# Performance work log

Measured on AMD Instinct MI355X. Metric: run time of the kernel, lower is better.

The kernel has to match this reference:

```python
import jax, jax.numpy as jnp
import numpy as np

N_NODES = 50000


def gcn_conv(x, W, b, src, dst, n_nodes):
    """PyG GCNConv: add self-loops, symmetric norm, linear, scatter-add, bias."""
    h = x @ W  # [N, out]
    # degree with self-loops: deg[i] = 1 + (# edges with dst == i)
    deg = 1.0 + jax.ops.segment_sum(jnp.ones_like(dst, dtype=h.dtype), dst,
                                    num_segments=n_nodes)
    dinv = jax.lax.rsqrt(deg)  # deg^{-1/2}
    # per-edge norm for non-self-loop edges
    norm = dinv[src] * dinv[dst]  # [E]
    agg = jax.ops.segment_sum(h[src] * norm[:, None], dst,
                              num_segments=n_nodes)
    # self-loop contribution: dinv[i]*dinv[i]*h[i] = h[i]/deg[i]
    agg = agg + h * (dinv * dinv)[:, None]
    return agg + b


def setup_inputs() -> dict:
    key = jax.random.key(0)
    ks = jax.random.split(key, 6)
    x = jax.random.normal(ks[0], (N_NODES, 512), dtype=jnp.float32)
    edge_index = jax.random.randint(ks[1], (2, 800000), 0, N_NODES,
                                    dtype=jnp.int64)
    W1 = jax.random.normal(ks[2], (512, 256), dtype=jnp.float32) * (512 ** -0.5)
    b1 = jnp.zeros((256,), dtype=jnp.float32)
    W2 = jax.random.normal(ks[3], (256, 256), dtype=jnp.float32) * (256 ** -0.5)
    b2 = jnp.zeros((256,), dtype=jnp.float32)
    W3 = jax.random.normal(ks[4], (256, 64), dtype=jnp.float32) * (256 ** -0.5)
    b3 = jnp.zeros((64,), dtype=jnp.float32)
    return {"x": x, "edge_index": edge_index, "W1": W1, "b1": b1,
            "W2": W2, "b2": b2, "W3": W3, "b3": b3}


def reference(x, edge_index, W1, b1, W2, b2, W3, b3):
    src, dst = edge_index[0], edge_index[1]
    n = x.shape[0]
    h = gcn_conv(x, W1, b1, src, dst, n)
    h = jax.nn.relu(h)  # dropout is a no-op in eval mode
    h = gcn_conv(h, W2, b2, src, dst, n)
    h = jax.nn.relu(h)
    h = gcn_conv(h, W3, b3, src, dst, n)
    # faithful to the original: softmax then log_softmax
    h = jax.nn.softmax(h, axis=1)
    return jax.nn.log_softmax(h, axis=1)
```

## Files before the change

### kernel.cpp

```cpp
#include <hip/hip_runtime.h>
#include <cstdint>
#include <cstddef>

typedef float  f32x4  __attribute__((ext_vector_type(4)));
typedef float  f32x2  __attribute__((ext_vector_type(2)));

__device__ __forceinline__ unsigned int f2fp8x4(float a, float b, float c, float d) {
  int v = __builtin_amdgcn_cvt_pk_fp8_f32(a, b, 0, false);
  v = __builtin_amdgcn_cvt_pk_fp8_f32(c, d, v, true);
  return (unsigned int)v;
}
__device__ __forceinline__ unsigned char f2fp8(float f) {
  return (unsigned char)(__builtin_amdgcn_cvt_pk_fp8_f32(f, f, 0, false) & 0xff);
}
__device__ __forceinline__ void fp8x8_to_f32(uint2 d, float* f) {
  f32x2 a = __builtin_amdgcn_cvt_pk_f32_fp8((int)d.x, false);
  f32x2 b = __builtin_amdgcn_cvt_pk_f32_fp8((int)d.x, true);
  f32x2 c = __builtin_amdgcn_cvt_pk_f32_fp8((int)d.y, false);
  f32x2 e = __builtin_amdgcn_cvt_pk_f32_fp8((int)d.y, true);
  f[0] = a.x; f[1] = a.y; f[2] = b.x; f[3] = b.y;
  f[4] = c.x; f[5] = c.y; f[6] = e.x; f[7] = e.y;
}
__device__ __forceinline__ void fp8x4_to_f32(unsigned int d, float* f) {
  f32x2 a = __builtin_amdgcn_cvt_pk_f32_fp8((int)d, false);
  f32x2 b = __builtin_amdgcn_cvt_pk_f32_fp8((int)d, true);
  f[0] = a.x; f[1] = a.y; f[2] = b.x; f[3] = b.y;
}
__device__ __forceinline__ void fp8x16_to_f32(uint4 d, float* f) {
  uint2 lo; lo.x = d.x; lo.y = d.y;
  uint2 hi; hi.x = d.z; hi.y = d.w;
  fp8x8_to_f32(lo, f);
  fp8x8_to_f32(hi, f + 8);
}

__device__ __forceinline__ void async_copy16(const void* g, void* l) {
  __builtin_amdgcn_global_load_lds(
      (const __attribute__((address_space(1))) unsigned int*)g,
      (__attribute__((address_space(3))) unsigned int*)l, 16, 0, 0);
}

#define NN 50000
#define MPAD 50048
#define SCAN_BLOCKS 196

#define XB_BLOCKS 6256
#define WB_BLOCKS 52

__global__ __launch_bounds__(256) void gcn_prep_k(
    const float* __restrict__ X, unsigned char* __restrict__ x8,
    const float* __restrict__ W1, const float* __restrict__ W2,
    const float* __restrict__ W3,
    unsigned char* __restrict__ W1T8, unsigned char* __restrict__ W2T8,
    unsigned char* __restrict__ W3T8, int* __restrict__ cnt) {
  int b = blockIdx.x;
  if (b < SCAN_BLOCKS) {
    int ii = b * 256 + threadIdx.x;
    if (ii < NN) cnt[ii] = 0;
  }
  if (b < XB_BLOCKS) {
    int idx16 = (b * 256 + threadIdx.x) * 16;
    int row = idx16 >> 9;
    uint4 o;
    if (row < NN) {
      const float* s = &X[idx16];
      float4 v0 = *(const float4*)s;
      float4 v1 = *(const float4*)(s + 4);
      float4 v2 = *(const float4*)(s + 8);
      float4 v3 = *(const float4*)(s + 12);
      o.x = f2fp8x4(v0.x, v0.y, v0.z, v0.w);
      o.y = f2fp8x4(v1.x, v1.y, v1.z, v1.w);
      o.z = f2fp8x4(v2.x, v2.y, v2.z, v2.w);
      o.w = f2fp8x4(v3.x, v3.y, v3.z, v3.w);
    } else {
      o = uint4{0, 0, 0, 0};
    }
    *(uint4*)&x8[idx16] = o;
  } else {
    int wb = b - XB_BLOCKS;
    if (wb < 32) {
      int idx16 = (wb * 256 + threadIdx.x) * 16;
      int n = idx16 >> 9;
      float f[16];
#pragma unroll
      for (int j = 0; j < 16; j++) f[j] = W1[(size_t)((idx16 & 511) + j) * 256 + n];
      uint4 o;
      o.x = f2fp8x4(f[0], f[1], f[2], f[3]);
      o.y = f2fp8x4(f[4], f[5], f[6], f[7]);
      o.z = f2fp8x4(f[8], f[9], f[10], f[11]);
      o.w = f2fp8x4(f[12], f[13], f[14], f[15]);
      *(uint4*)&W1T8[idx16] = o;
    } else if (wb < 48) {
      int idx16 = ((wb - 32) * 256 + threadIdx.x) * 16;
      int n = idx16 >> 8;
      float f[16];
#pragma unroll
      for (int j = 0; j < 16; j++) f[j] = W2[(size_t)((idx16 & 255) + j) * 256 + n];
      uint4 o;
      o.x = f2fp8x4(f[0], f[1], f[2], f[3]);
      o.y = f2fp8x4(f[4], f[5], f[6], f[7]);
      o.z = f2fp8x4(f[8], f[9], f[10], f[11]);
      o.w = f2fp8x4(f[12], f[13], f[14], f[15]);
      *(uint4*)&W2T8[idx16] = o;
    } else {
      int idx16 = ((wb - 48) * 256 + threadIdx.x) * 16;
      int n = idx16 >> 8;
      float f[16];
#pragma unroll
      for (int j = 0; j < 16; j++) f[j] = W3[(size_t)((idx16 & 255) + j) * 64 + n];
      uint4 o;
      o.x = f2fp8x4(f[0], f[1], f[2], f[3]);
      o.y = f2fp8x4(f[4], f[5], f[6], f[7]);
      o.z = f2fp8x4(f[8], f[9], f[10], f[11]);
      o.w = f2fp8x4(f[12], f[13], f[14], f[15]);
      *(uint4*)&W3T8[idx16] = o;
    }
  }
}

__global__ void gcn_count_k(const int* __restrict__ dst, int* __restrict__ cnt,
                            int* __restrict__ rank, int E) {
  int e = blockIdx.x * 256 + threadIdx.x;
  if (e < E) rank[e] = atomicAdd(&cnt[dst[e]], 1);
}

__global__ __launch_bounds__(256) void gcn_scan_blocks_k(
    const int* __restrict__ cnt, int* __restrict__ blockSum, int nNodes) {
  __shared__ int sw[4];
  int t = threadIdx.x;
  int i = blockIdx.x * 256 + t;
  int v = (i < nNodes) ? cnt[i] : 0;
  for (int off = 32; off > 0; off >>= 1) v += __shfl_down(v, off);
  if ((t & 63) == 0) sw[t >> 6] = v;
  __syncthreads();
  if (t == 0) blockSum[blockIdx.x] = sw[0] + sw[1] + sw[2] + sw[3];
}

__global__ __launch_bounds__(256) void gcn_scan_tops_k(
    int* __restrict__ blockSum, int nBlocks) {
  __shared__ int sb[256];
  int t = threadIdx.x;
  int v = (t < nBlocks) ? blockSum[t] : 0;
  sb[t] = v;
  __syncthreads();
  for (int off = 1; off < 256; off <<= 1) {
    int x = (t >= off) ? sb[t - off] : 0;
    __syncthreads();
    sb[t] += x;
    __syncthreads();
  }
  if (t < nBlocks) blockSum[t] = sb[t] - v;
}

__global__ __launch_bounds__(256) void gcn_scan_final_k(
    const int* __restrict__ cnt, const int* __restrict__ blockSum,
    int* __restrict__ rs, float* __restrict__ dinv, int nNodes, int E) {
  __shared__ int sb[256];
  int t = threadIdx.x;
  int i = blockIdx.x * 256 + t;
  int v = (i < nNodes) ? cnt[i] : 0;
  sb[t] = v;
  __syncthreads();
  for (int off = 1; off < 256; off <<= 1) {
    int x = (t >= off) ? sb[t - off] : 0;
    __syncthreads();
    sb[t] += x;
    __syncthreads();
  }
  if (i < nNodes) {
    rs[i] = blockSum[blockIdx.x] + sb[t] - v;
    dinv[i] = rsqrtf(1.0f + (float)v);
  } else if (i < MPAD) {
    dinv[i] = 0.0f;
  }
  if (i == 0) rs[nNodes] = E;
}

__global__ void gcn_scatter_k(const int* __restrict__ src, const int* __restrict__ dst,
                              const int* __restrict__ rank, const int* __restrict__ rs,
                              int* __restrict__ e4, int E) {
  int e = blockIdx.x * 256 + threadIdx.x;
  if (e < E) {
    int d = dst[e];
    e4[rs[d] + rank[e]] = src[e];
  }
}

template<int BN, int WTN>
__global__ __launch_bounds__(256) void gcn_gemm_f8_db_k(
    const unsigned char* __restrict__ A8,
    const unsigned char* __restrict__ Bt8,
    const float* __restrict__ dinv,
    unsigned char* __restrict__ C8,
    int K, int N) {
  static_assert(BN == 128, "db kernel assumes uniform 2 global_load_lds per thread");
  __shared__ __align__(16) unsigned char lds_a[2][128 * 32];
  __shared__ __align__(16) unsigned char lds_b[2][BN * 32];
  const int t = threadIdx.x;
  const int wave = t >> 6, lane = t & 63;
  const int wr = wave >> 1, wc = wave & 1;
  const int quad = lane >> 4, lrow = lane & 15;
  const int m0 = blockIdx.x * 128;
  const int n0 = blockIdx.y * BN;

  f32x4 acc[4][WTN] = {};

  auto stage = [&](int buf, int k0) {
    int r = t >> 1, c = (t & 1) * 16;
    async_copy16(&A8[(size_t)(m0 + r) * K + k0 + c], &lds_a[buf][t * 16]);
    async_copy16(&Bt8[(size_t)(n0 + r) * K + k0 + c], &lds_b[buf][t * 16]);
  };
  auto compute = [&](int buf) {
    long af[4], bfr[WTN];
#pragma unroll
    for (int mt = 0; mt < 4; mt++)
      af[mt] = *(const long*)&lds_a[buf][(wr * 64 + mt * 16 + lrow) * 32 + quad * 8];
#pragma unroll
    for (int nt = 0; nt < WTN; nt++)
      bfr[nt] = *(const long*)&lds_b[buf][(wc * (BN / 2) + nt * 16 + lrow) * 32 + quad * 8];
#pragma unroll
    for (int mt = 0; mt < 4; mt++)
#pragma unroll
      for (int nt = 0; nt < WTN; nt++)
        acc[mt][nt] = __builtin_amdgcn_mfma_f32_16x16x32_fp8_fp8(af[mt], bfr[nt], acc[mt][nt], 0, 0, 0);
  };

  stage(0, 0);
  int curb = 0;
  int k0 = 0;
  for (; k0 + 32 < K; k0 += 32) {
    stage(curb ^ 1, k0 + 32);
    asm volatile("s_waitcnt vmcnt(2)" ::: "memory");
    __builtin_amdgcn_s_barrier();
    asm volatile("" ::: "memory");
    compute(curb);
    asm volatile("" ::: "memory");
    __builtin_amdgcn_s_barrier();
    curb ^= 1;
  }
  asm volatile("s_waitcnt vmcnt(0)" ::: "memory");
  __builtin_amdgcn_s_barrier();
  asm volatile("" ::: "memory");
  compute(curb);

#pragma unroll
  for (int mt = 0; mt < 4; mt++)
#pragma unroll
    for (int r = 0; r < 4; r++) {
      int row = m0 + wr * 64 + mt * 16 + quad * 4 + r;
      float dv = dinv[row];
#pragma unroll
      for (int nt = 0; nt < WTN; nt++) {
        int col = n0 + wc * (BN / 2) + nt * 16 + lrow;
        C8[(size_t)row * N + col] = f2fp8(acc[mt][nt][r] * dv);
      }
    }
}

template<int BN, int WTN>
__global__ __launch_bounds__(256) void gcn_gemm_f8_s_k(
    const unsigned char* __restrict__ A8, const unsigned char* __restrict__ Bt8,
    const float* __restrict__ dinv, unsigned char* __restrict__ C8, int K, int N) {
  __shared__ __align__(16) unsigned char lds_a[128 * 32];
  __shared__ __align__(16) unsigned char lds_b[BN * 32];
  const int t = threadIdx.x;
  const int wave = t >> 6, lane = t & 63;
  const int wr = wave >> 1, wc = wave & 1;
  const int quad = lane >> 4, lrow = lane & 15;
  const int m0 = blockIdx.x * 128;
  const int n0 = blockIdx.y * BN;

  f32x4 acc[4][WTN] = {};

  for (int k0 = 0; k0 < K; k0 += 32) {
    __syncthreads();
    {
      int r = t >> 1, c = (t & 1) * 16;
      async_copy16(&A8[(size_t)(m0 + r) * K + k0 + c], &lds_a[t * 16]);
    }
    for (int q = t; q < BN * 2; q += 256) {
      int r = q >> 1, c = (q & 1) * 16;
      async_copy16(&Bt8[(size_t)(n0 + r) * K + k0 + c], &lds_b[q * 16]);
    }
    __syncthreads();
    long af[4], bfr[WTN];
#pragma unroll
    for (int mt = 0; mt < 4; mt++)
      af[mt] = *(const long*)&lds_a[(wr * 64 + mt * 16 + lrow) * 32 + quad * 8];
#pragma unroll
    for (int nt = 0; nt < WTN; nt++)
      bfr[nt] = *(const long*)&lds_b[(wc * (BN / 2) + nt * 16 + lrow) * 32 + quad * 8];
#pragma unroll
    for (int mt = 0; mt < 4; mt++)
#pragma unroll
      for (int nt = 0; nt < WTN; nt++)
        acc[mt][nt] = __builtin_amdgcn_mfma_f32_16x16x32_fp8_fp8(af[mt], bfr[nt], acc[mt][nt], 0, 0, 0);
  }

#pragma unroll
  for (int mt = 0; mt < 4; mt++)
#pragma unroll
    for (int r = 0; r < 4; r++) {
      int row = m0 + wr * 64 + mt * 16 + quad * 4 + r;
      float dv = dinv[row];
#pragma unroll
      for (int nt = 0; nt < WTN; nt++) {
        int col = n0 + wc * (BN / 2) + nt * 16 + lrow;
        C8[(size_t)row * N + col] = f2fp8(acc[mt][nt][r] * dv);
      }
    }
}

template<int D>
__global__ __launch_bounds__(256) void gcn_agg_relu_k(
    const unsigned char* __restrict__ g8, const int* __restrict__ rs,
    const int* __restrict__ e4, const float* __restrict__ dinv,
    const float* __restrict__ bias, unsigned char* __restrict__ out8, int nNodes) {
  int wave = threadIdx.x >> 6, lane = threadIdx.x & 63;
  int i = blockIdx.x * 4 + wave;
  if (i >= nNodes) return;
  int q = lane >> 4, sub = lane & 15;
  int f0 = sub * 16;
  float di = dinv[i];
  uint4 dself = *(const uint4*)&g8[(size_t)i * D + f0];
  float sv[16];
  fp8x16_to_f32(dself, sv);
  float wself = (q == 0) ? 1.0f : 0.0f;
  float acc[16];
#pragma unroll
  for (int j = 0; j < 16; j++) acc[j] = sv[j] * wself;

  int e0 = rs[i], e1 = rs[i + 1];
  int nIter = (e1 - e0 + 15) >> 4;
  int e = e0 + q;
  for (int k = 0; k < nIter; k++) {
    int idx[4]; float w[4];
#pragma unroll
    for (int u = 0; u < 4; u++) {
      int ee = e + 4 * u;
      bool v = ee < e1;
      idx[u] = v ? e4[ee] : 0;
      w[u] = v ? 1.0f : 0.0f;
    }
    uint4 d0 = *(const uint4*)&g8[(size_t)idx[0] * D + f0];
    uint4 d1 = *(const uint4*)&g8[(size_t)idx[1] * D + f0];
    uint4 d2 = *(const uint4*)&g8[(size_t)idx[2] * D + f0];
    uint4 d3 = *(const uint4*)&g8[(size_t)idx[3] * D + f0];
    float r[16];
    fp8x16_to_f32(d0, r);
#pragma unroll
    for (int j = 0; j < 16; j++) acc[j] += r[j] * w[0];
    fp8x16_to_f32(d1, r);
#pragma unroll
    for (int j = 0; j < 16; j++) acc[j] += r[j] * w[1];
    fp8x16_to_f32(d2, r);
#pragma unroll
    for (int j = 0; j < 16; j++) acc[j] += r[j] * w[2];
    fp8x16_to_f32(d3, r);
#pragma unroll
    for (int j = 0; j < 16; j++) acc[j] += r[j] * w[3];
    e += 16;
  }
#pragma unroll
  for (int j = 0; j < 16; j++) {
    acc[j] += __shfl_xor(acc[j], 16);
    acc[j] += __shfl_xor(acc[j], 32);
  }
  if (q == 0) {
    float4 bb0 = *(const float4*)&bias[f0];
    float4 bb1 = *(const float4*)&bias[f0 + 4];
    float4 bb2 = *(const float4*)&bias[f0 + 8];
    float4 bb3 = *(const float4*)&bias[f0 + 12];
    float bv[16] = {bb0.x, bb0.y, bb0.z, bb0.w, bb1.x, bb1.y, bb1.z, bb1.w,
                    bb2.x, bb2.y, bb2.z, bb2.w, bb3.x, bb3.y, bb3.z, bb3.w};
    float r[16];
#pragma unroll
    for (int j = 0; j < 16; j++) {
      float z = di * acc[j] + bv[j];
      r[j] = z > 0.0f ? z : 0.0f;
    }
    uint4 o;
    o.x = f2fp8x4(r[0], r[1], r[2], r[3]);
    o.y = f2fp8x4(r[4], r[5], r[6], r[7]);
    o.z = f2fp8x4(r[8], r[9], r[10], r[11]);
    o.w = f2fp8x4(r[12], r[13], r[14], r[15]);
    *(uint4*)&out8[(size_t)i * D + f0] = o;
  }
}

__global__ __launch_bounds__(256) void gcn_agg_final_k(
    const unsigned char* __restrict__ g8, const int* __restrict__ rs,
    const int* __restrict__ e4, const float* __restrict__ dinv,
    const float* __restrict__ bias, float* __restrict__ out, int nNodes) {
  int wave = threadIdx.x >> 6, lane = threadIdx.x & 63;
  int i = blockIdx.x * 4 + wave;
  if (i >= nNodes) return;
  int qtr = lane >> 4, sub = lane & 15;
  int f0 = sub * 4;
  float di = dinv[i];
  unsigned int dself = *(const unsigned int*)&g8[(size_t)i * 64 + f0];
  float sv[4];
  fp8x4_to_f32(dself, sv);
  float wself = (qtr == 0) ? 1.0f : 0.0f;
  float acc[4];
#pragma unroll
  for (int j = 0; j < 4; j++) acc[j] = sv[j] * wself;

  int e0 = rs[i], e1 = rs[i + 1];
  int nIter = (e1 - e0 + 7) >> 3;
  int e = e0 + qtr;
  for (int k = 0; k < nIter; k++) {
    int idx[2]; float w[2];
#pragma unroll
    for (int u = 0; u < 2; u++) {
      int ee = e + 4 * u;
      bool v = ee < e1;
      idx[u] = v ? e4[ee] : 0;
      w[u] = v ? 1.0f : 0.0f;
    }
    unsigned int d0 = *(const unsigned int*)&g8[(size_t)idx[0] * 64 + f0];
    unsigned int d1 = *(const unsigned int*)&g8[(size_t)idx[1] * 64 + f0];
    float r0[4], r1[4];
    fp8x4_to_f32(d0, r0); fp8x4_to_f32(d1, r1);
#pragma unroll
    for (int j = 0; j < 4; j++)
      acc[j] += r0[j] * w[0] + r1[j] * w[1];
    e += 8;
  }
#pragma unroll
  for (int j = 0; j < 4; j++) {
    acc[j] += __shfl_xor(acc[j], 16);
    acc[j] += __shfl_xor(acc[j], 32);
    acc[j] = di * acc[j] + bias[f0 + j];
  }
  float m = fmaxf(fmaxf(acc[0], acc[1]), fmaxf(acc[2], acc[3]));
#pragma unroll
  for (int off = 8; off > 0; off >>= 1) m = fmaxf(m, __shfl_xor(m, off));
  float ex[4], s = 0.0f;
#pragma unroll
  for (int j = 0; j < 4; j++) { ex[j] = __expf(acc[j] - m); s += ex[j]; }
#pragma unroll
  for (int off = 8; off > 0; off >>= 1) s += __shfl_xor(s, off);
  float rcs = 1.0f / s;
  float p[4], s2 = 0.0f;
#pragma unroll
  for (int j = 0; j < 4; j++) { p[j] = ex[j] * rcs; s2 += __expf(p[j]); }
#pragma unroll
  for (int off = 8; off > 0; off >>= 1) s2 += __shfl_xor(s2, off);
  float ls = __logf(s2);
  if (qtr == 0) {
    float4 o; o.x = p[0] - ls; o.y = p[1] - ls; o.z = p[2] - ls; o.w = p[3] - ls;
    *(float4*)&out[(size_t)i * 64 + f0] = o;
  }
}

extern "C" void kernel_launch(void* const* d_in, const int* in_sizes, int n_in,
                              void* d_out, int out_size, void* d_ws, size_t ws_size,
                              hipStream_t stream) {
  const float* x    = (const float*)d_in[0];
  const int*   eidx = (const int*)d_in[1];
  const float* W1   = (const float*)d_in[2];
  const float* b1   = (const float*)d_in[3];
  const float* W2   = (const float*)d_in[4];
  const float* b2   = (const float*)d_in[5];
  const float* W3   = (const float*)d_in[6];
  const float* b3   = (const float*)d_in[7];
  float* out = (float*)d_out;

  const int E = in_sizes[1] / 2;
  const int* src = eidx;
  const int* dst = eidx + E;

  char* p = (char*)d_ws;
  auto alloc = [&](size_t bytes) -> void* {
    void* r = (void*)p;
    p += (bytes + 255) & ~(size_t)255;
    return r;
  };
  unsigned char*  x8   = (unsigned char*)alloc((size_t)MPAD * 512);
  unsigned char*  g8   = (unsigned char*)alloc((size_t)MPAD * 256);
  unsigned char*  a8   = (unsigned char*)alloc((size_t)MPAD * 256);
  unsigned char*  g83  = (unsigned char*)alloc((size_t)MPAD * 64);
  unsigned char*  W1T8 = (unsigned char*)alloc((size_t)256 * 512);
  unsigned char*  W2T8 = (unsigned char*)alloc((size_t)256 * 256);
  unsigned char*  W3T8 = (unsigned char*)alloc((size_t)64 * 256);
  int*   cnt  = (int*)alloc((size_t)NN * 4);
  int*   rs   = (int*)alloc((size_t)(NN + 1) * 4);
  int*   rank = (int*)alloc((size_t)E * 4);
  float* dinv = (float*)alloc((size_t)MPAD * 4);
  int*   e4   = (int*)alloc((size_t)(E + 64) * 4);
  int*   bsum = (int*)alloc((size_t)SCAN_BLOCKS * 4);

  const int EB = (E + 255) / 256;
  gcn_prep_k<<<XB_BLOCKS + WB_BLOCKS, 256, 0, stream>>>(
      x, x8, W1, W2, W3, W1T8, W2T8, W3T8, cnt);
  gcn_count_k<<<EB, 256, 0, stream>>>(dst, cnt, rank, E);
  gcn_scan_blocks_k<<<SCAN_BLOCKS, 256, 0, stream>>>(cnt, bsum, NN);
  gcn_scan_tops_k<<<1, 256, 0, stream>>>(bsum, SCAN_BLOCKS);
  gcn_scan_final_k<<<SCAN_BLOCKS, 256, 0, stream>>>(cnt, bsum, rs, dinv, NN, E);
  gcn_scatter_k<<<EB, 256, 0, stream>>>(src, dst, rank, rs, e4, E);

  const int MB = MPAD / 128;
  gcn_gemm_f8_db_k<128, 4><<<dim3(MB, 2), 256, 0, stream>>>(x8, W1T8, dinv, g8, 512, 256);
  gcn_agg_relu_k<256><<<(NN + 3) / 4, 256, 0, stream>>>(g8, rs, e4, dinv, b1, a8, NN);
  gcn_gemm_f8_db_k<128, 4><<<dim3(MB, 2), 256, 0, stream>>>(a8, W2T8, dinv, g8, 256, 256);
  gcn_agg_relu_k<256><<<(NN + 3) / 4, 256, 0, stream>>>(g8, rs, e4, dinv, b2, a8, NN);
  gcn_gemm_f8_s_k<64, 2><<<dim3(MB, 1), 256, 0, stream>>>(a8, W3T8, dinv, g83, 256, 64);
  gcn_agg_final_k<<<(NN + 3) / 4, 256, 0, stream>>>(g83, rs, e4, dinv, b3, out, NN);

  (void)n_in; (void)out_size; (void)ws_size;
}
```

Measured before the change: 406.7 us.

## Fuse first GEMM with edge-count kernel and fold top-level scan into final scan

The first-layer GEMM no longer depends on dinv: the source-side dinv scaling moves into the first aggregation kernel, which now reads dinv per neighbour. That lets GEMM1 run in the same launch as the edge-degree atomic counting, so compute-heavy and atomic-heavy blocks share the GPU. The single-block top-level scan kernel is removed, and every final-scan block instead re-scans the block sums redundantly. The cost is an extra dinv gather per edge in layer-1 aggregation and duplicated scan work in each block.

```diff
diff --git a/kernel.cpp b/kernel.cpp
--- a/kernel.cpp
+++ b/kernel.cpp
@@ -45,6 +45,9 @@
 
 #define XB_BLOCKS 6256
 #define WB_BLOCKS 52
+
+#define GEMM1_BLOCKS 782
+#define COUNT_BLOCKS 3125
 
 __global__ __launch_bounds__(256) void gcn_prep_k(
     const float* __restrict__ X, unsigned char* __restrict__ x8,
@@ -117,10 +120,77 @@
   }
 }
 
-__global__ void gcn_count_k(const int* __restrict__ dst, int* __restrict__ cnt,
-                            int* __restrict__ rank, int E) {
-  int e = blockIdx.x * 256 + threadIdx.x;
-  if (e < E) rank[e] = atomicAdd(&cnt[dst[e]], 1);
+__global__ __launch_bounds__(256) void gcn_gemm1_count_k(
+    const unsigned char* __restrict__ A8,
+    const unsigned char* __restrict__ Bt8,
+    unsigned char* __restrict__ C8,
+    const int* __restrict__ dst, int* __restrict__ cnt, int* __restrict__ rank, int E) {
+  __shared__ __align__(16) unsigned char lds_a[2][128 * 32];
+  __shared__ __align__(16) unsigned char lds_b[2][128 * 32];
+  int b = blockIdx.x;
+  if (b >= GEMM1_BLOCKS) {
+    int e = (b - GEMM1_BLOCKS) * 256 + threadIdx.x;
+    if (e < E) rank[e] = atomicAdd(&cnt[dst[e]], 1);
+    return;
+  }
+  const int K = 512, N = 256;
+  const int t = threadIdx.x;
+  const int wave = t >> 6, lane = t & 63;
+  const int wr = wave >> 1, wc = wave & 1;
+  const int quad = lane >> 4, lrow = lane & 15;
+  const int m0 = (b >> 1) * 128;
+  const int n0 = (b & 1) * 128;
+
+  f32x4 acc[4][4] = {};
+
+  auto stage = [&](int buf, int k0) {
+    int r = t >> 1, c = (t & 1) * 16;
+    async_copy16(&A8[(size_t)(m0 + r) * K + k0 + c], &lds_a[buf][t * 16]);
+    async_copy16(&Bt8[(size_t)(n0 + r) * K + k0 + c], &lds_b[buf][t * 16]);
+  };
+  auto compute = [&](int buf) {
+    long af[4], bfr[4];
+#pragma unroll
+    for (int mt = 0; mt < 4; mt++)
+      af[mt] = *(const long*)&lds_a[buf][(wr * 64 + mt * 16 + lrow) * 32 + quad * 8];
+#pragma unroll
+    for (int nt = 0; nt < 4; nt++)
+      bfr[nt] = *(const long*)&lds_b[buf][(wc * 64 + nt * 16 + lrow) * 32 + quad * 8];
+#pragma unroll
+    for (int mt = 0; mt < 4; mt++)
+#pragma unroll
+      for (int nt = 0; nt < 4; nt++)
+        acc[mt][nt] = __builtin_amdgcn_mfma_f32_16x16x32_fp8_fp8(af[mt], bfr[nt], acc[mt][nt], 0, 0, 0);
+  };
+
+  stage(0, 0);
+  int curb = 0;
+  int k0 = 0;
+  for (; k0 + 32 < K; k0 += 32) {
+    stage(curb ^ 1, k0 + 32);
+    asm volatile("s_waitcnt vmcnt(2)" ::: "memory");
+    __builtin_amdgcn_s_barrier();
+    asm volatile("" ::: "memory");
+    compute(curb);
+    asm volatile("" ::: "memory");
+    __builtin_amdgcn_s_barrier();
+    curb ^= 1;
+  }
+  asm volatile("s_waitcnt vmcnt(0)" ::: "memory");
+  __builtin_amdgcn_s_barrier();
+  asm volatile("" ::: "memory");
+  compute(curb);
+
+#pragma unroll
+  for (int mt = 0; mt < 4; mt++)
+#pragma unroll
+    for (int nt = 0; nt < 4; nt++)
+#pragma unroll
+      for (int r = 0; r < 4; r++) {
+        int row = m0 + wr * 64 + mt * 16 + quad * 4 + r;
+        int col = n0 + wc * 64 + nt * 16 + lrow;
+        C8[(size_t)row * N + col] = f2fp8(acc[mt][nt][r]);
+      }
 }
 
 __global__ __launch_bounds__(256) void gcn_scan_blocks_k(
@@ -135,39 +205,29 @@
   if (t == 0) blockSum[blockIdx.x] = sw[0] + sw[1] + sw[2] + sw[3];
 }
 
-__global__ __launch_bounds__(256) void gcn_scan_tops_k(
-    int* __restrict__ blockSum, int nBlocks) {
-  __shared__ int sb[256];
-  int t = threadIdx.x;
-  int v = (t < nBlocks) ? blockSum[t] : 0;
-  sb[t] = v;
-  __syncthreads();
-  for (int off = 1; off < 256; off <<= 1) {
-    int x = (t >= off) ? sb[t - off] : 0;
-    __syncthreads();
-    sb[t] += x;
-    __syncthreads();
-  }
-  if (t < nBlocks) blockSum[t] = sb[t] - v;
-}
-
 __global__ __launch_bounds__(256) void gcn_scan_final_k(
     const int* __restrict__ cnt, const int* __restrict__ blockSum,
     int* __restrict__ rs, float* __restrict__ dinv, int nNodes, int E) {
   __shared__ int sb[256];
+  __shared__ int sc[256];
   int t = threadIdx.x;
   int i = blockIdx.x * 256 + t;
   int v = (i < nNodes) ? cnt[i] : 0;
   sb[t] = v;
+  int w = (t < SCAN_BLOCKS) ? blockSum[t] : 0;
+  sc[t] = w;
   __syncthreads();
   for (int off = 1; off < 256; off <<= 1) {
     int x = (t >= off) ? sb[t - off] : 0;
+    int y = (t >= off) ? sc[t - off] : 0;
     __syncthreads();
     sb[t] += x;
+    sc[t] += y;
     __syncthreads();
   }
+  int base = sc[blockIdx.x] - blockSum[blockIdx.x];
   if (i < nNodes) {
-    rs[i] = blockSum[blockIdx.x] + sb[t] - v;
+    rs[i] = base + sb[t] - v;
     dinv[i] = rsqrtf(1.0f + (float)v);
   } else if (i < MPAD) {
     dinv[i] = 0.0f;
@@ -310,7 +370,7 @@
     }
 }
 
-template<int D>
+template<int D, int WSRC>
 __global__ __launch_bounds__(256) void gcn_agg_relu_k(
     const unsigned char* __restrict__ g8, const int* __restrict__ rs,
     const int* __restrict__ e4, const float* __restrict__ dinv,
@@ -324,7 +384,7 @@
   uint4 dself = *(const uint4*)&g8[(size_t)i * D + f0];
   float sv[16];
   fp8x16_to_f32(dself, sv);
-  float wself = (q == 0) ? 1.0f : 0.0f;
+  float wself = (q == 0) ? (WSRC ? di : 1.0f) : 0.0f;
   float acc[16];
 #pragma unroll
   for (int j = 0; j < 16; j++) acc[j] = sv[j] * wself;
@@ -339,7 +399,7 @@
       int ee = e + 4 * u;
       bool v = ee < e1;
       idx[u] = v ? e4[ee] : 0;
-      w[u] = v ? 1.0f : 0.0f;
+      w[u] = v ? (WSRC ? dinv[idx[u]] : 1.0f) : 0.0f;
     }
     uint4 d0 = *(const uint4*)&g8[(size_t)idx[0] * D + f0];
     uint4 d1 = *(const uint4*)&g8[(size_t)idx[1] * D + f0];
@@ -493,17 +553,15 @@
   const int EB = (E + 255) / 256;
   gcn_prep_k<<<XB_BLOCKS + WB_BLOCKS, 256, 0, stream>>>(
       x, x8, W1, W2, W3, W1T8, W2T8, W3T8, cnt);
-  gcn_count_k<<<EB, 256, 0, stream>>>(dst, cnt, rank, E);
+  gcn_gemm1_count_k<<<GEMM1_BLOCKS + COUNT_BLOCKS, 256, 0, stream>>>(
+      x8, W1T8, g8, dst, cnt, rank, E);
   gcn_scan_blocks_k<<<SCAN_BLOCKS, 256, 0, stream>>>(cnt, bsum, NN);
-  gcn_scan_tops_k<<<1, 256, 0, stream>>>(bsum, SCAN_BLOCKS);
   gcn_scan_final_k<<<SCAN_BLOCKS, 256, 0, stream>>>(cnt, bsum, rs, dinv, NN, E);
   gcn_scatter_k<<<EB, 256, 0, stream>>>(src, dst, rank, rs, e4, E);
-
+  gcn_agg_relu_k<256, 1><<<(NN + 3) / 4, 256, 0, stream>>>(g8, rs, e4, dinv, b1, a8, NN);
   const int MB = MPAD / 128;
-  gcn_gemm_f8_db_k<128, 4><<<dim3(MB, 2), 256, 0, stream>>>(x8, W1T8, dinv, g8, 512, 256);
-  gcn_agg_relu_k<256><<<(NN + 3) / 4, 256, 0, stream>>>(g8, rs, e4, dinv, b1, a8, NN);
   gcn_gemm_f8_db_k<128, 4><<<dim3(MB, 2), 256, 0, stream>>>(a8, W2T8, dinv, g8, 256, 256);
-  gcn_agg_relu_k<256><<<(NN + 3) / 4, 256, 0, stream>>>(g8, rs, e4, dinv, b2, a8, NN);
+  gcn_agg_relu_k<256, 0><<<(NN + 3) / 4, 256, 0, stream>>>(g8, rs, e4, dinv, b2, a8, NN);
   gcn_gemm_f8_s_k<64, 2><<<dim3(MB, 1), 256, 0, stream>>>(a8, W3T8, dinv, g83, 256, 64);
   gcn_agg_final_k<<<(NN + 3) / 4, 256, 0, stream>>>(g83, rs, e4, dinv, b3, out, NN);
 
```

New measurement: 385.1 us. -5.3%, faster.
